# Performance work log

Hardware: AMD Instinct MI355X
Metric: run time of the kernel (lower is better)

The kernel has to match this reference:

```python
import jax, jax.numpy as jnp
import numpy as np

N_QUBITS = 10
DEPTH = 2
CNOT_PATTERN = [(i, i + 1) for i in range(N_QUBITS - 1)] + [(N_QUBITS - 1, 0)]

def _signs(n):
    # Pauli-Z eigenvalue (+1/-1) of each basis state for each wire; wire 0 = MSB
    idx = np.arange(2 ** n)
    bits = (idx[:, None] >> np.arange(n - 1, -1, -1)[None, :]) & 1
    return jnp.asarray(1.0 - 2.0 * bits, jnp.float32)  # [2^n, n]

SIGNS = _signs(N_QUBITS)

def _apply_rx(s, theta, wire):
    # s: [B, 2,2,...,2] complex; RX(theta) = [[c, -i s],[-i s, c]], c=cos(theta/2)
    s0 = jnp.take(s, 0, axis=wire + 1)
    s1 = jnp.take(s, 1, axis=wire + 1)
    c = jnp.cos(theta * 0.5)
    sn = jnp.sin(theta * 0.5)
    if c.ndim:  # per-batch angle -> broadcast over remaining wire axes
        shp = (-1,) + (1,) * (s0.ndim - 1)
        c = c.reshape(shp)
        sn = sn.reshape(shp)
    return jnp.stack([c * s0 - 1j * sn * s1, -1j * sn * s0 + c * s1], axis=wire + 1)

def _apply_cnot(s, src, tgt):
    # flip target wire on the src=1 subspace (X gate == flip of the size-2 axis)
    s0 = jnp.take(s, 0, axis=src + 1)
    s1 = jnp.take(s, 1, axis=src + 1)
    t_ax = tgt + 1 - (1 if tgt > src else 0)  # target axis after removing src axis
    s1 = jnp.flip(s1, axis=t_ax)
    return jnp.stack([s0, s1], axis=src + 1)

def _qgate(x, rx_params):
    # x: [B, n_qubits] data angles -> PauliZ expectations [B, n_qubits]
    B = x.shape[0]
    n = N_QUBITS
    s = jnp.zeros((B, 2 ** n), jnp.complex64).at[:, 0].set(1.0)
    s = s.reshape((B,) + (2,) * n)
    for w in range(n):
        s = _apply_rx(s, x[:, w], w)
    for _ in range(DEPTH):
        for w in range(n):
            s = _apply_rx(s, rx_params[w], w)
        for src, tgt in CNOT_PATTERN:
            s = _apply_cnot(s, src, tgt)
    probs = jnp.abs(s.reshape(B, -1)) ** 2  # [B, 2^n]
    return probs @ SIGNS  # [B, n]


def setup_inputs():
    key = jax.random.key(0)
    ks = jax.random.split(key, 10)
    T, B, D, H = 256, 256, 128, N_QUBITS
    fan_in = D + H
    sc = 1.0 / np.sqrt(fan_in)
    def lin(k1, k2):
        W = jax.random.uniform(k1, (H, fan_in), jnp.float32, -sc, sc)
        b = jax.random.uniform(k2, (H,), jnp.float32, -sc, sc)
        return W, b
    inputs = jax.random.normal(ks[0], (T, B, D), jnp.float32)
    rx_params = jax.random.normal(ks[1], (H,), jnp.float32)
    Wf, bf = lin(ks[2], ks[3])
    Wi, bi = lin(ks[4], ks[5])
    Wg, bg = lin(ks[6], ks[7])
    Wo, bo = lin(ks[8], ks[9])
    return dict(inputs=inputs, rx_params=rx_params, Wf=Wf, bf=bf, Wi=Wi, bi=bi,
                Wg=Wg, bg=bg, Wo=Wo, bo=bo)


def reference(inputs, rx_params, Wf, bf, Wi, bi, Wg, bg, Wo, bo):
    T, B, _ = inputs.shape
    H = N_QUBITS
    def step(carry, x_t):
        hx, cx = carry
        comb = jnp.concatenate([x_t, hx], axis=1)  # [B, D+H]
        f = jax.nn.sigmoid(_qgate(comb @ Wf.T + bf, rx_params))
        i = jax.nn.sigmoid(_qgate(comb @ Wi.T + bi, rx_params))
        g = jnp.tanh(_qgate(comb @ Wg.T + bg, rx_params))
        o = jax.nn.sigmoid(_qgate(comb @ Wo.T + bo, rx_params))
        cx = f * cx + i * g
        hx = o * jnp.tanh(cx)
        return (hx, cx), hx
    h0 = jnp.zeros((B, H), inputs.dtype)
    c0 = jnp.zeros((B, H), inputs.dtype)
    (hT, cT), ys = jax.lax.scan(step, (h0, c0), inputs)
    return ys, hT, cT
```

## Files before the change

### kernel.cpp

```cpp
#include <hip/hip_runtime.h>
#include <math.h>

#define T_STEPS 256
#define BATCH   256
#define DDIM    128
#define NH      10

typedef float v2f __attribute__((ext_vector_type(2)));
__device__ __forceinline__ v2f sp(float x){ v2f r; r.x = x; r.y = x; return r; }
#define PKFMA(a,b,c) __builtin_elementwise_fma((a),(b),(c))

template<int CTRL, int RMASK, int BMASK>
__device__ __forceinline__ float dppz(float x){
  return __int_as_float(__builtin_amdgcn_update_dpp(
      0, __float_as_int(x), CTRL, RMASK, BMASK, true));
}
template<int CTRL>
__device__ __forceinline__ float qperm(float x){
  int xi = __float_as_int(x);
  return __int_as_float(__builtin_amdgcn_update_dpp(xi, xi, CTRL, 0xF, 0xF, false));
}
__device__ __forceinline__ float rdlane(float v, int l){
  return __int_as_float(__builtin_amdgcn_readlane(__float_as_int(v), l));
}
__device__ __forceinline__ float qp2(float x){ return qperm<0x4E>(x); }
__device__ __forceinline__ float qp1(float x){ return qperm<0xB1>(x); }
__device__ __forceinline__ float lane_xor4(float x){
  int xi = __float_as_int(x);
  int t = __builtin_amdgcn_update_dpp(xi, xi, 0x104, 0xF, 0x5, false);
  t     = __builtin_amdgcn_update_dpp(t,  xi, 0x114, 0xF, 0xA, false);
  return __int_as_float(t);
}
__device__ __forceinline__ float lane_xor8(float x){
  int xi = __float_as_int(x);
  int t = __builtin_amdgcn_update_dpp(xi, xi, 0x108, 0xF, 0x3, false);
  t     = __builtin_amdgcn_update_dpp(t,  xi, 0x118, 0xF, 0xC, false);
  return __int_as_float(t);
}

template<int CTRL,int RMASK,int BMASK>
__device__ __forceinline__ float lad_add(float v){ return v + dppz<CTRL,RMASK,BMASK>(v); }
template<int CTRL,int RMASK,int BMASK>
__device__ __forceinline__ float lad_sub(float v){ return dppz<CTRL,RMASK,BMASK>(v) - v; }
#define LAD0_A(v) lad_add<0x111,0xF,0xF>(v)
#define LAD0_S(v) lad_sub<0x111,0xF,0xF>(v)
#define LAD1_A(v) lad_add<0x112,0xF,0xF>(v)
#define LAD1_S(v) lad_sub<0x112,0xF,0xF>(v)
#define LAD2_A(v) lad_add<0x114,0xF,0xE>(v)
#define LAD2_S(v) lad_sub<0x114,0xF,0xE>(v)
#define LAD3_A(v) lad_add<0x118,0xF,0xC>(v)
#define LAD3_S(v) lad_sub<0x118,0xF,0xC>(v)
#define LAD4_A(v) lad_add<0x142,0xA,0xF>(v)
#define LAD4_S(v) lad_sub<0x142,0xA,0xF>(v)
#define LAD5_A(v) lad_add<0x143,0xC,0xF>(v)
#define LAD5_S(v) lad_sub<0x143,0xC,0xF>(v)

__device__ __forceinline__ float dsx32(float x){ return __shfl_xor(x, 32, 64); }
__device__ __forceinline__ float dsx16(float x){
  return __int_as_float(__builtin_amdgcn_ds_swizzle(__float_as_int(x), 0x401F));
}
__device__ __forceinline__ float bperm(int addr, float v){
  return __int_as_float(__builtin_amdgcn_ds_bpermute(addr, __float_as_int(v)));
}

#define NK 4

#define RX_LANE_T(FETCH, tv)                                                   \
  { const v2f tt_ = sp(tv), nt_ = sp(-(tv));                                   \
    _Pragma("unroll")                                                          \
    for (int k = 0; k < NK; ++k){                                              \
      v2f oa, ob;                                                              \
      oa.x = FETCH(RE[k].x); oa.y = FETCH(RE[k].y);                            \
      ob.x = FETCH(IM[k].x); ob.y = FETCH(IM[k].y);                            \
      RE[k] = PKFMA(tt_, ob, RE[k]);                                           \
      IM[k] = PKFMA(nt_, oa, IM[k]);                                           \
    } }

template<int XB>
__device__ __forceinline__ void rx_reg_t(float tv, v2f* RE, v2f* IM){
  const v2f tt = sp(tv), nt = sp(-tv);
  v2f oR[NK], oI[NK];
  #pragma unroll
  for (int k = 0; k < NK; ++k){ oR[k] = RE[k]; oI[k] = IM[k]; }
  #pragma unroll
  for (int k = 0; k < NK; ++k){
    RE[k] = PKFMA(tt, oI[k ^ XB], RE[k]);
    IM[k] = PKFMA(nt, oR[k ^ XB], IM[k]);
  }
}
__device__ __forceinline__ void rx_reg9_t(float tv, v2f* RE, v2f* IM){
  const v2f tt = sp(tv), nt = sp(-tv);
  #pragma unroll
  for (int k = 0; k < NK; ++k){
    v2f oa = __builtin_shufflevector(RE[k], RE[k], 1, 0);
    v2f ob = __builtin_shufflevector(IM[k], IM[k], 1, 0);
    RE[k] = PKFMA(tt, ob, RE[k]);
    IM[k] = PKFMA(nt, oa, IM[k]);
  }
}

__device__ __forceinline__ void xdots5(float xa, float xb,
                                       const v2f* WA, const v2f* WB,
                                       int l5, int l4, int l3, float* s){
  v2f xav = sp(xa), xbv = sp(xb);
  v2f p0 = PKFMA(xav, WA[0], xbv * WB[0]);
  v2f p1 = PKFMA(xav, WA[1], xbv * WB[1]);
  v2f p2 = PKFMA(xav, WA[2], xbv * WB[2]);
  float a  = p0.x + dsx32(p0.x);
  float bv = p0.y + dsx32(p0.y);
  float c  = p1.x + dsx32(p1.x);
  float d  = p1.y + dsx32(p1.y);
  float e  = p2.x + dsx32(p2.x);
  float m1 = l5 ? bv : a;
  float m2 = l5 ? d : c;
  m1 += dsx16(m1);
  m2 += dsx16(m2);
  e  += dsx16(e);
  float n1 = l4 ? m2 : m1;
  n1 += lane_xor8(n1);
  e  += lane_xor8(e);
  float p = l3 ? e : n1;
  p += lane_xor4(p);
  p += qp2(p);
  p += qp1(p);
  s[0] = rdlane(p, 0);
  s[1] = rdlane(p, 32);
  s[2] = rdlane(p, 16);
  s[3] = rdlane(p, 48);
  s[4] = rdlane(p, 8);
}

__global__ void __launch_bounds__(512)
__attribute__((amdgpu_waves_per_eu(2)))
qlstm_kernel(const float* __restrict__ inp, const float* __restrict__ rxp,
             const float* __restrict__ Wf, const float* __restrict__ bf,
             const float* __restrict__ Wi, const float* __restrict__ bi,
             const float* __restrict__ Wg, const float* __restrict__ bg,
             const float* __restrict__ Wo, const float* __restrict__ bo,
             float* __restrict__ out)
{
  const int b    = blockIdx.x;
  const int tid  = threadIdx.x;
  const int wv   = tid >> 6;
  const int g    = wv >> 1;
  const int half = wv & 1;
  const int lane = tid & 63;

  __shared__ float4 partv[2][64];
  __shared__ float xpub_s[4][16];
  ((float*)partv)[tid] = 0.f;
  if (tid < 64) ((float*)xpub_s)[tid] = 0.f;

  const float* Wp = (g == 0) ? Wf : (g == 1) ? Wi : (g == 2) ? Wg : Wo;
  const float* bp = (g == 0) ? bf : (g == 1) ? bi : (g == 2) ? bg : bo;

  const float WSC = 0.07957747154594767f;

  const int wbase = half * 5;
  v2f WA[3], WB[3];
  float bq[5];
  #pragma unroll
  for (int k = 0; k < 5; ++k) bq[k] = WSC * (bp[wbase + k] + rxp[wbase + k]);
  #pragma unroll
  for (int j = 0; j < 3; ++j){
    const int w0 = wbase + 2*j, w1 = wbase + 2*j + 1;
    WA[j].x = WSC * Wp[w0*138 + lane];
    WB[j].x = WSC * Wp[w0*138 + 64 + lane];
    if (2*j + 1 < 5){
      WA[j].y = WSC * Wp[w1*138 + lane];
      WB[j].y = WSC * Wp[w1*138 + 64 + lane];
    } else { WA[j].y = 0.f; WB[j].y = 0.f; }
  }
  const int trigAct = (lane < NH) || (lane >= 16 && lane < 16 + NH);
  float wCT[NH];
  {
    const int row = trigAct ? (lane & 15) : 0;
    #pragma unroll
    for (int j = 0; j < NH; ++j){
      float v = WSC * Wp[row*138 + 128 + j];
      wCT[j] = trigAct ? v : 0.f;
    }
  }
  const float shift = ((lane >> 4) & 1) ? -0.25f : 0.f;

  float tq[NH];
  float PC = 1.f;
  #pragma unroll
  for (int w = 0; w < NH; ++w){
    float th = 0.5f * rxp[w];
    float cw = cosf(th), sw = sinf(th);
    PC *= cw;
    tq[w] = sw / cw;
  }

  const int l5 = (lane>>5)&1, l4 = (lane>>4)&1, l3 = (lane>>3)&1;
  const int l2 = (lane>>2)&1, l1 = (lane>>1)&1, l0 = lane&1;
  const int pb2 = l4^l3, pb3 = l3^l2, pb4 = l2^l1, pb5 = l1^l0;
  const int a0 = l5, a1 = l5^l4;
  const int a6w = l0 ^ half;
  const int n_base = pb2 + pb3 + pb4 + pb5 + a6w;

  const int adF2  = 4*(2 + 16*pb2);
  const int adF3  = 4*(3 + 16*pb3);
  const int adF4  = 4*(4 + 16*pb4);
  const int adF5  = 4*(5 + 16*pb5);
  const int adW6o = 4*(6 + 16*a6w);
  const int adW6p = 4*(6 + 16*(a6w^1));
  const int adQ0a = 4*(0 + 16*a0);
  const int adQ0b = 4*(1 + 16*a1);
  const int adQ1a = 4*(0 + 16*(a0^1));
  const int adQ1b = 4*(1 + 16*(a1^1));

  v2f CRE[NK], CIM[NK], D6RE[NK], D6IM[NK];
  #pragma unroll
  for (int r = 0; r < 2*NK; ++r){
    const int R0 = r&1, R1 = (r>>1)&1, R2 = (r>>2)&1;
    int k = (n_base + (a0^R0) + (a1^R0) + (half^R2) + (R2^R1) + (R1^R0)) & 3;
    float cr = (k==0) ? PC : (k==2) ? -PC : 0.f;
    float ci = (k==1) ? -PC : (k==3) ? PC : 0.f;
    float sg6 = ((l0 ^ R2) & 1) ? tq[6] : -tq[6];
    float dre = sg6 * ci;
    float dim = -sg6 * cr;
    if (R0){ CRE[r>>1].y = cr;  CIM[r>>1].y = ci;
             D6RE[r>>1].y = dre; D6IM[r>>1].y = dim; }
    else   { CRE[r>>1].x = cr;  CIM[r>>1].x = ci;
             D6RE[r>>1].x = dre; D6IM[r>>1].x = dim; }
  }

  const float sig = (lane == 0 || lane >= 6) ? -1.f : 1.f;

  float h = 0.f, c = 0.f;

  const float* x0 = inp + (size_t)b * DDIM;
  float xa = x0[lane];
  float xb = x0[64 + lane];

  {
    float sx[5];
    xdots5(xa, xb, WA, WB, l5, l4, l3, sx);
    if (lane == 63){
      #pragma unroll
      for (int k = 0; k < 5; ++k) xpub_s[g][wbase + k] = sx[k] + bq[k];
    }
  }
  __syncthreads();

  #pragma unroll 1
  for (int t = 0; t < T_STEPS; ++t){
    if (t + 1 < T_STEPS){
      const float* nx = inp + ((size_t)(t+1) * BATCH + b) * DDIM;
      xa = nx[lane];
      xb = nx[64 + lane];
    }

    float cA;
    {
      float xr = xpub_s[g][lane & 15];
      float hdA = rdlane(h, 0) * wCT[0];
      float hdB = rdlane(h, 1) * wCT[1];
      hdA = fmaf(rdlane(h, 2), wCT[2], hdA);
      hdB = fmaf(rdlane(h, 3), wCT[3], hdB);
      hdA = fmaf(rdlane(h, 4), wCT[4], hdA);
      hdB = fmaf(rdlane(h, 5), wCT[5], hdB);
      hdA = fmaf(rdlane(h, 6), wCT[6], hdA);
      hdB = fmaf(rdlane(h, 7), wCT[7], hdB);
      hdA = fmaf(rdlane(h, 8), wCT[8], hdA);
      hdB = fmaf(rdlane(h, 9), wCT[9], hdB);
      float th = (xr + (hdA + hdB)) + shift;
      cA = __builtin_amdgcn_cosf(th);
    }

    float f2  = bperm(adF2,  cA);
    float f3  = bperm(adF3,  cA);
    float f4  = bperm(adF4,  cA);
    float f5  = bperm(adF5,  cA);
    float w6o = bperm(adW6o, cA);
    float w6p = bperm(adW6p, cA);
    float q0a = bperm(adQ0a, cA);
    float q0b = bperm(adQ0b, cA);
    float q1a = bperm(adQ1a, cA);
    float q1b = bperm(adQ1b, cA);
    float m2345b = (f2*f3)*(f4*f5);
    float mo = m2345b * w6o;
    float mp = m2345b * w6p;
    float q0 = q0a*q0b, q1 = q1a*q1b;
    v2f ZZ; ZZ.x = mo * q0; ZZ.y = mo * q1;
    v2f ZP; ZP.x = mp * q0; ZP.y = mp * q1;

    float u7  = rdlane(cA, 7 + 16*half);
    float u7b = rdlane(cA, 23 - 16*half);
    float c8  = rdlane(cA, 8);
    float s8  = rdlane(cA, 24);
    float c9  = rdlane(cA, 9);
    float s9  = rdlane(cA, 25);
    float t78[4];
    t78[0] = u7  * c8;
    t78[1] = u7  * s8;
    t78[2] = u7b * s8;
    t78[3] = u7b * c8;
    v2f s9a; s9a.x = c9; s9a.y = s9;
    v2f s9b; s9b.x = s9; s9b.y = c9;

    v2f RE[NK], IM[NK];
    #pragma unroll
    for (int k = 0; k < NK; ++k){
      v2f s9v = (k & 1) ? s9b : s9a;
      v2f M  = (sp(t78[k])     * s9v) * ZZ;
      v2f Mp = (sp(t78[k ^ 3]) * s9v) * ZP;
      RE[k] = PKFMA(Mp, D6RE[k], M * CRE[k]);
      IM[k] = PKFMA(Mp, D6IM[k], M * CIM[k]);
    }

    RX_LANE_T(dsx32, tq[0])
    rx_reg_t<2>(tq[7], RE, IM);
    RX_LANE_T(dsx16, tq[1])
    rx_reg_t<1>(tq[8], RE, IM);
    RX_LANE_T(lane_xor8, tq[2])
    rx_reg9_t  (tq[9], RE, IM);
    RX_LANE_T(lane_xor4, tq[3])
    RX_LANE_T(qp2, tq[4])
    RX_LANE_T(qp1, tq[5])

    float sx[5];
    xdots5(xa, xb, WA, WB, l5, l4, l3, sx);

    v2f Pk[NK];
    #pragma unroll
    for (int k = 0; k < NK; ++k) Pk[k] = PKFMA(RE[k], RE[k], IM[k] * IM[k]);
    float A0 = Pk[0].x + Pk[0].y, A1 = Pk[1].x + Pk[1].y;
    float A2 = Pk[2].x + Pk[2].y, A3 = Pk[3].x + Pk[3].y;
    float B0 = Pk[0].x - Pk[0].y, B1 = Pk[1].x - Pk[1].y;
    float B2 = Pk[2].x - Pk[2].y, B3 = Pk[3].x - Pk[3].y;
    float su = A0 + A1, sv = A2 + A3;
    float tot = su + sv;
    float q4  = su - sv;
    float q6  = (A0 - A1) - (A2 - A3);
    float q7  = (B0 - B1) - (B2 - B3);

    float a0p = LAD0_A(tot);
    float a0m = LAD0_S(tot);
    float b1pp = LAD1_A(a0p);
    float b1pm = LAD1_S(a0p);
    float b1mm = LAD1_S(a0m);
    float c2ppp = LAD2_A(b1pp);
    float c2ppm = LAD2_S(b1pp);
    float c2pmm = LAD2_S(b1pm);
    float c2mmm = LAD2_S(b1mm);
    float d1 = LAD3_A(c2ppp);
    float d2 = LAD3_S(c2ppp);
    float d3 = LAD3_S(c2ppm);
    float d4 = LAD3_S(c2pmm);
    float d5 = LAD3_S(c2mmm);
    float P1 = LAD5_S(LAD4_S(d1));
    float P2 = LAD5_S(LAD4_S(d2));
    float P3 = LAD5_S(LAD4_S(d3));
    float P4 = LAD5_S(LAD4_S(d4));
    float P5 = LAD5_S(LAD4_S(d5));
    float e = LAD0_S(q7);
    e = LAD1_S(e); e = LAD2_S(e); e = LAD3_S(e); e = LAD4_S(e);
    float P9 = LAD5_S(e);
    float P0 = LAD5_A(e);
    float f_ = LAD0_S(q4);
    f_ = LAD1_S(f_); f_ = LAD2_S(f_); f_ = LAD3_S(f_); f_ = LAD4_S(f_);
    float P7 = LAD5_S(f_);
    float g_ = LAD0_S(q6);
    g_ = LAD1_S(g_); g_ = LAD2_S(g_); g_ = LAD3_S(g_); g_ = LAD4_S(g_);
    float P8 = LAD5_S(g_);

    if (lane == 63){
      float vals[10] = {P0,P1,P2,P3,P4,P5,P5,P7,P8,P9};
      #pragma unroll
      for (int j = 0; j < 10; ++j)
        ((float*)&partv[half][j])[g] = vals[j];
      #pragma unroll
      for (int k = 0; k < 5; ++k)
        xpub_s[g][wbase + k] = sx[k] + bq[k];
    }
    __syncthreads();

    float4 eL = partv[0][lane];
    float4 eH = partv[1][lane];
    float E0 = fmaf(sig, eH.x, eL.x);
    float E1 = fmaf(sig, eH.y, eL.y);
    float E2 = fmaf(sig, eH.z, eL.z);
    float E3 = fmaf(sig, eH.w, eL.w);
    float fv = 1.f / (1.f + __expf(-E0));
    float iv = 1.f / (1.f + __expf(-E1));
    float e2g = __expf(2.f * E2);
    float gv = (e2g - 1.f) / (e2g + 1.f);
    float ov = 1.f / (1.f + __expf(-E3));
    c = fmaf(fv, c, iv * gv);
    float e2c = __expf(2.f * c);
    h = ov * ((e2c - 1.f) / (e2c + 1.f));

    if (wv == 0 && lane < NH)
      out[((size_t)t * BATCH + b) * NH + lane] = h;
  }

  if (wv == 0 && lane < NH){
    const size_t ysN = (size_t)T_STEPS * BATCH * NH;
    out[ysN + (size_t)b * NH + lane]                      = h;
    out[ysN + (size_t)BATCH * NH + (size_t)b * NH + lane] = c;
  }
}

extern "C" void kernel_launch(void* const* d_in, const int* in_sizes, int n_in,
                              void* d_out, int out_size, void* d_ws, size_t ws_size,
                              hipStream_t stream)
{
  qlstm_kernel<<<BATCH, 512, 0, stream>>>(
      (const float*)d_in[0], (const float*)d_in[1],
      (const float*)d_in[2], (const float*)d_in[3],
      (const float*)d_in[4], (const float*)d_in[5],
      (const float*)d_in[6], (const float*)d_in[7],
      (const float*)d_in[8], (const float*)d_in[9],
      (float*)d_out);
}
```

Baseline: 782.6 us.

## Fold wire-0 RX into initial state build and replace bpermutes with readlanes

Replaces the ten ds_bpermute gathers of per-wire cos/sin values with fourteen scalar readlanes plus per-lane selects. It also folds the first parametrised RX on wire 0, previously a cross-lane dsx32 exchange, into the analytic initial-state construction. This uses precomputed D0 and D60 coefficient tables and swapped ZZ/ZP products. The aim is to remove LDS-path permute latency and one full cross-lane RX stage from the serial per-step chain, at the cost of more registers and a few extra packed FMAs.

```diff
diff --git a/kernel.cpp b/kernel.cpp
--- a/kernel.cpp
+++ b/kernel.cpp
@@ -58,9 +58,6 @@
 __device__ __forceinline__ float dsx32(float x){ return __shfl_xor(x, 32, 64); }
 __device__ __forceinline__ float dsx16(float x){
   return __int_as_float(__builtin_amdgcn_ds_swizzle(__float_as_int(x), 0x401F));
-}
-__device__ __forceinline__ float bperm(int addr, float v){
-  return __int_as_float(__builtin_amdgcn_ds_bpermute(addr, __float_as_int(v)));
 }
 
 #define NK 4
@@ -200,31 +197,28 @@
   const int a6w = l0 ^ half;
   const int n_base = pb2 + pb3 + pb4 + pb5 + a6w;
 
-  const int adF2  = 4*(2 + 16*pb2);
-  const int adF3  = 4*(3 + 16*pb3);
-  const int adF4  = 4*(4 + 16*pb4);
-  const int adF5  = 4*(5 + 16*pb5);
-  const int adW6o = 4*(6 + 16*a6w);
-  const int adW6p = 4*(6 + 16*(a6w^1));
-  const int adQ0a = 4*(0 + 16*a0);
-  const int adQ0b = 4*(1 + 16*a1);
-  const int adQ1a = 4*(0 + 16*(a0^1));
-  const int adQ1b = 4*(1 + 16*(a1^1));
-
   v2f CRE[NK], CIM[NK], D6RE[NK], D6IM[NK];
+  v2f D0RE[NK], D0IM[NK], D60RE[NK], D60IM[NK];
   #pragma unroll
   for (int r = 0; r < 2*NK; ++r){
     const int R0 = r&1, R1 = (r>>1)&1, R2 = (r>>2)&1;
     int k = (n_base + (a0^R0) + (a1^R0) + (half^R2) + (R2^R1) + (R1^R0)) & 3;
     float cr = (k==0) ? PC : (k==2) ? -PC : 0.f;
     float ci = (k==1) ? -PC : (k==3) ? PC : 0.f;
-    float sg6 = ((l0 ^ R2) & 1) ? tq[6] : -tq[6];
-    float dre = sg6 * ci;
-    float dim = -sg6 * cr;
-    if (R0){ CRE[r>>1].y = cr;  CIM[r>>1].y = ci;
-             D6RE[r>>1].y = dre; D6IM[r>>1].y = dim; }
-    else   { CRE[r>>1].x = cr;  CIM[r>>1].x = ci;
-             D6RE[r>>1].x = dre; D6IM[r>>1].x = dim; }
+    float s6s = ((l0 ^ R2) & 1) ? 1.f : -1.f;
+    float s0s = l4 ? 1.f : -1.f;
+    float d6re =  tq[6]*s6s*ci,  d6im = -tq[6]*s6s*cr;
+    float d0re =  tq[0]*s0s*ci,  d0im = -tq[0]*s0s*cr;
+    float t60  = -tq[6]*tq[0]*s6s*s0s;
+    float d60re = t60*cr, d60im = t60*ci;
+    if (R0){ CRE[r>>1].y = cr;   CIM[r>>1].y = ci;
+             D6RE[r>>1].y = d6re; D6IM[r>>1].y = d6im;
+             D0RE[r>>1].y = d0re; D0IM[r>>1].y = d0im;
+             D60RE[r>>1].y = d60re; D60IM[r>>1].y = d60im; }
+    else   { CRE[r>>1].x = cr;   CIM[r>>1].x = ci;
+             D6RE[r>>1].x = d6re; D6IM[r>>1].x = d6im;
+             D0RE[r>>1].x = d0re; D0IM[r>>1].x = d0im;
+             D60RE[r>>1].x = d60re; D60IM[r>>1].x = d60im; }
   }
 
   const float sig = (lane == 0 || lane >= 6) ? -1.f : 1.f;
@@ -270,22 +264,28 @@
       cA = __builtin_amdgcn_cosf(th);
     }
 
-    float f2  = bperm(adF2,  cA);
-    float f3  = bperm(adF3,  cA);
-    float f4  = bperm(adF4,  cA);
-    float f5  = bperm(adF5,  cA);
-    float w6o = bperm(adW6o, cA);
-    float w6p = bperm(adW6p, cA);
-    float q0a = bperm(adQ0a, cA);
-    float q0b = bperm(adQ0b, cA);
-    float q1a = bperm(adQ1a, cA);
-    float q1b = bperm(adQ1b, cA);
+    float cs0 = rdlane(cA, 0), sn0 = rdlane(cA, 16);
+    float cs1 = rdlane(cA, 1), sn1 = rdlane(cA, 17);
+    float cs2 = rdlane(cA, 2), sn2 = rdlane(cA, 18);
+    float cs3 = rdlane(cA, 3), sn3 = rdlane(cA, 19);
+    float cs4 = rdlane(cA, 4), sn4 = rdlane(cA, 20);
+    float cs5 = rdlane(cA, 5), sn5 = rdlane(cA, 21);
+    float cs6 = rdlane(cA, 6), sn6 = rdlane(cA, 22);
+    float f2  = pb2 ? sn2 : cs2;
+    float f3  = pb3 ? sn3 : cs3;
+    float f4  = pb4 ? sn4 : cs4;
+    float f5  = pb5 ? sn5 : cs5;
+    float w6o = a6w ? sn6 : cs6;
+    float w6p = a6w ? cs6 : sn6;
+    float q0  = (a0 ? sn0 : cs0) * (a1 ? sn1 : cs1);
+    float q1  = (a0 ? cs0 : sn0) * (a1 ? cs1 : sn1);
     float m2345b = (f2*f3)*(f4*f5);
     float mo = m2345b * w6o;
     float mp = m2345b * w6p;
-    float q0 = q0a*q0b, q1 = q1a*q1b;
     v2f ZZ; ZZ.x = mo * q0; ZZ.y = mo * q1;
     v2f ZP; ZP.x = mp * q0; ZP.y = mp * q1;
+    v2f ZZs = __builtin_shufflevector(ZZ, ZZ, 1, 0);
+    v2f ZPs = __builtin_shufflevector(ZP, ZP, 1, 0);
 
     float u7  = rdlane(cA, 7 + 16*half);
     float u7b = rdlane(cA, 23 - 16*half);
@@ -305,15 +305,22 @@
     #pragma unroll
     for (int k = 0; k < NK; ++k){
       v2f s9v = (k & 1) ? s9b : s9a;
-      v2f M  = (sp(t78[k])     * s9v) * ZZ;
-      v2f Mp = (sp(t78[k ^ 3]) * s9v) * ZP;
-      RE[k] = PKFMA(Mp, D6RE[k], M * CRE[k]);
-      IM[k] = PKFMA(Mp, D6IM[k], M * CIM[k]);
-    }
-
-    RX_LANE_T(dsx32, tq[0])
+      v2f G   = sp(t78[k])     * s9v;
+      v2f Gp  = sp(t78[k ^ 3]) * s9v;
+      v2f M   = G  * ZZ;
+      v2f Mp6 = Gp * ZP;
+      v2f M0  = G  * ZZs;
+      v2f M60 = Gp * ZPs;
+      RE[k] = PKFMA(M60, D60RE[k],
+              PKFMA(M0,  D0RE[k],
+              PKFMA(Mp6, D6RE[k], M * CRE[k])));
+      IM[k] = PKFMA(M60, D60IM[k],
+              PKFMA(M0,  D0IM[k],
+              PKFMA(Mp6, D6IM[k], M * CIM[k])));
+    }
+
+    RX_LANE_T(dsx16, tq[1])
     rx_reg_t<2>(tq[7], RE, IM);
-    RX_LANE_T(dsx16, tq[1])
     rx_reg_t<1>(tq[8], RE, IM);
     RX_LANE_T(lane_xor8, tq[2])
     rx_reg9_t  (tq[9], RE, IM);
```

After: 755.0 us (median of 2 runs). -3.5%, faster.
